# Optimization experiments

Hardware: AMD Instinct MI355X
Metric: run time of the kernel (lower is better)

## Reference

```python
import jax, jax.numpy as jnp
import numpy as np

EPS = 1e-9
N_HEAD = 16


def clamp_c(c):
    return jnp.clip(c, 1e-4, 1.0)


def _heads(x, H):
    B, T, C = x.shape
    return x.reshape(B, T, H, C // H)


def mobius_add(x, y, c_clamped, H):
    # per-head Mobius addition; c_clamped: (H,)
    B, T, C = x.shape
    cr = c_clamped.reshape(1, 1, H, 1)
    xr, yr = _heads(x, H), _heads(y, H)
    xn = jnp.sum(xr * xr, axis=-1, keepdims=True)
    yn = jnp.sum(yr * yr, axis=-1, keepdims=True)
    ip = jnp.sum(xr * yr, axis=-1, keepdims=True)
    num = (1 + 2 * cr * ip + cr * yn) * xr + (1 - cr * xn) * yr
    den = 1 + 2 * cr * ip + cr ** 2 * xn * yn
    return (num / (den + EPS)).reshape(B, T, C)


def expmap(x, v, c, H):
    # exponential map of tangent vector v at point x (per-head curvature)
    B, T, C = x.shape
    cc = clamp_c(c)
    cr = cc.reshape(1, 1, H, 1)
    xr, vr = _heads(x, H), _heads(v, H)
    sf = 2.0 / (1 + cr * jnp.sum(xr * xr, axis=-1, keepdims=True) + EPS)  # scaling factor
    vns = jnp.sum(vr * vr, axis=-1, keepdims=True)
    vn = jnp.sqrt(vns + EPS)
    tanh_arg = jnp.abs(cr * sf * vns / 2)
    coeff = (1.0 / (jnp.sqrt(jnp.abs(cr) + EPS) + EPS)) * jnp.tanh(jnp.sqrt(tanh_arg + EPS))
    second = (coeff * vr / (vn + EPS)).reshape(B, T, C)
    return mobius_add(x, second, cc, H)


def layernorm(x, g):
    m = jnp.mean(x, axis=-1, keepdims=True)
    v = jnp.mean((x - m) ** 2, axis=-1, keepdims=True)
    return (x - m) * jax.lax.rsqrt(v + 1e-5) * g


def attention(x, w_qkv, w_proj, H):
    B, T, C = x.shape
    hs = C // H
    q, k, v = jnp.split(x @ w_qkv.T, 3, axis=-1)
    q = q.reshape(B, T, H, hs).transpose(0, 2, 1, 3)
    k = k.reshape(B, T, H, hs).transpose(0, 2, 1, 3)
    v = v.reshape(B, T, H, hs).transpose(0, 2, 1, 3)
    att = jnp.einsum('bhqd,bhkd->bhqk', q, k) * (float(hs) ** -0.5)
    mask = jnp.tril(jnp.ones((T, T), dtype=bool))
    att = jnp.where(mask, att, -jnp.inf)
    att = jax.nn.softmax(att, axis=-1)
    y = jnp.einsum('bhqk,bhkd->bhqd', att, v)
    y = y.transpose(0, 2, 1, 3).reshape(B, T, C)
    return y @ w_proj.T


def setup_inputs() -> dict:
    key = jax.random.key(0)
    ks = jax.random.split(key, 9)
    B, T, C = 2, 2048, 1024
    s = 0.02
    return {
        'x': jax.random.normal(ks[0], (B, T, C), jnp.float32) * s,
        'ln1_g': jnp.ones((C,), jnp.float32),
        'w_qkv': jax.random.normal(ks[1], (3 * C, C), jnp.float32) * s,
        'w_attn_proj': jax.random.normal(ks[2], (C, C), jnp.float32) * s,
        'c_attn': jax.random.uniform(ks[3], (N_HEAD,), jnp.float32, 0.1, 0.9),
        'ln2_g': jnp.ones((C,), jnp.float32),
        'w_fc': jax.random.normal(ks[4], (4 * C, C), jnp.float32) * s,
        'w_mlp_proj': jax.random.normal(ks[5], (C, 4 * C), jnp.float32) * s,
        'c_mlp': jax.random.uniform(ks[6], (N_HEAD,), jnp.float32, 0.1, 0.9),
    }


def reference(x, ln1_g, w_qkv, w_attn_proj, c_attn, ln2_g, w_fc, w_mlp_proj, c_mlp):
    H = N_HEAD
    a = attention(layernorm(x, ln1_g), w_qkv, w_attn_proj, H)
    x = expmap(x, a, c_attn, H)  # hyperbolic residual (attn)
    h = jax.nn.gelu(layernorm(x, ln2_g) @ w_fc.T, approximate=False) @ w_mlp_proj.T
    x = expmap(x, h, c_mlp, H)   # hyperbolic residual (mlp)
    return x
```

## Files before the change

kernel.cpp:

```cpp
#include <hip/hip_runtime.h>
#include <hip/hip_bf16.h>

typedef __attribute__((ext_vector_type(8))) short bf16x8;
typedef __attribute__((ext_vector_type(4))) float f32x4;

typedef const __attribute__((address_space(1))) void gv_t;
typedef __attribute__((address_space(3))) void lv_t;
#define GLL16(g, l) __builtin_amdgcn_global_load_lds((gv_t*)(g), (lv_t*)(l), 16, 0, 0)

__device__ __forceinline__ short f2bf(float f) {
    __hip_bfloat16 h = __float2bfloat16(f);
    return *reinterpret_cast<short*>(&h);
}

__device__ __forceinline__ float wred(float v) {
    #pragma unroll
    for (int m = 1; m < 64; m <<= 1) v += __shfl_xor(v, m);
    return v;
}

__global__ __launch_bounds__(256) void cvt_kernel(const float* __restrict__ in,
                                                  short* __restrict__ out, int n4) {
    int i = blockIdx.x * 256 + threadIdx.x;
    if (i < n4) {
        float4 v = ((const float4*)in)[i];
        short4 o;
        o.x = f2bf(v.x); o.y = f2bf(v.y); o.z = f2bf(v.z); o.w = f2bf(v.w);
        ((short4*)out)[i] = o;
    }
}

__global__ __launch_bounds__(256) void ln_kernel(const float* __restrict__ x,
                                                 const float* __restrict__ g,
                                                 short* __restrict__ y) {
    const int row = blockIdx.x, tid = threadIdx.x;
    const float4 v = ((const float4*)(x + (size_t)row * 1024))[tid];
    float s = v.x + v.y + v.z + v.w;
    float s2 = v.x * v.x + v.y * v.y + v.z * v.z + v.w * v.w;
    #pragma unroll
    for (int m = 1; m < 64; m <<= 1) { s += __shfl_xor(s, m); s2 += __shfl_xor(s2, m); }
    __shared__ float rs[4], rs2[4];
    if ((tid & 63) == 0) { rs[tid >> 6] = s; rs2[tid >> 6] = s2; }
    __syncthreads();
    s = rs[0] + rs[1] + rs[2] + rs[3];
    s2 = rs2[0] + rs2[1] + rs2[2] + rs2[3];
    const float mean = s * (1.0f / 1024.0f);
    const float var = s2 * (1.0f / 1024.0f) - mean * mean;
    const float r = rsqrtf(var + 1e-5f);
    const float4 gg = ((const float4*)g)[tid];
    short4 o;
    o.x = f2bf((v.x - mean) * r * gg.x);
    o.y = f2bf((v.y - mean) * r * gg.y);
    o.z = f2bf((v.z - mean) * r * gg.z);
    o.w = f2bf((v.w - mean) * r * gg.w);
    ((short4*)y)[(size_t)row * 256 + tid] = o;
}

template <int EPI>
__global__ __launch_bounds__(256, 2) void gemm_bt(const short* __restrict__ A,
                                                  const short* __restrict__ Bw,
                                                  int M, int N, int K,
                                                  void* __restrict__ o0,
                                                  void* __restrict__ o1,
                                                  void* __restrict__ o2) {
    __shared__ __align__(16) short As[128 * 32];
    __shared__ __align__(16) short Bs[128 * 32];
    const int tid = threadIdx.x;
    const int wid = tid >> 6, lane = tid & 63;
    const int wm = wid >> 1, wn = wid & 1;
    const int col = lane & 15, grp = lane >> 4;
    const int m0 = blockIdx.x * 128, n0 = blockIdx.y * 128;
    f32x4 acc[4][4] = {};
    const int rowA = tid >> 2;
    const int kc = (tid & 3) * 8;
    const short* ga = A + (size_t)(m0 + rowA) * K + kc;
    const short* gb = Bw + (size_t)(n0 + rowA) * K + kc;
    short* lA = As + wid * 512;
    short* lB = Bs + wid * 512;
    for (int k0 = 0; k0 < K; k0 += 32) {
        GLL16(ga + k0, lA);
        GLL16(ga + k0 + (size_t)64 * K, lA + 2048);
        GLL16(gb + k0, lB);
        GLL16(gb + k0 + (size_t)64 * K, lB + 2048);
        __syncthreads();
        bf16x8 af[4], bfr[4];
        #pragma unroll
        for (int i = 0; i < 4; ++i) {
            af[i] = *(const bf16x8*)&As[(wm * 64 + i * 16 + col) * 32 + grp * 8];
            bfr[i] = *(const bf16x8*)&Bs[(wn * 64 + i * 16 + col) * 32 + grp * 8];
        }
        #pragma unroll
        for (int mi = 0; mi < 4; ++mi)
            #pragma unroll
            for (int ni = 0; ni < 4; ++ni)
                acc[mi][ni] = __builtin_amdgcn_mfma_f32_16x16x32_bf16(af[mi], bfr[ni], acc[mi][ni], 0, 0, 0);
        __syncthreads();
    }
    #pragma unroll
    for (int mi = 0; mi < 4; ++mi) {
        #pragma unroll
        for (int ni = 0; ni < 4; ++ni) {
            #pragma unroll
            for (int i = 0; i < 4; ++i) {
                const int m = m0 + wm * 64 + mi * 16 + grp * 4 + i;
                const int n = n0 + wn * 64 + ni * 16 + col;
                const float v = acc[mi][ni][i];
                if (EPI == 0) {
                    const int b = m >> 11, t = m & 2047;
                    const int which = n >> 10, nn = n & 1023;
                    const int h = nn >> 6, d = nn & 63;
                    const size_t bh = (size_t)(b * 16 + h);
                    if (which == 0)
                        ((short*)o0)[(bh * 2048 + t) * 64 + d] = f2bf(v * 0.125f);
                    else if (which == 1)
                        ((short*)o1)[(bh * 2048 + t) * 64 + d] = f2bf(v);
                    else
                        ((short*)o2)[(bh * 64 + d) * 2048 + t] = f2bf(v);
                } else if (EPI == 1) {
                    ((float*)o0)[(size_t)m * N + n] = v;
                } else {
                    const float gl = 0.5f * v * (1.0f + erff(v * 0.70710678118654752f));
                    ((short*)o0)[(size_t)m * N + n] = f2bf(gl);
                }
            }
        }
    }
}

__global__ __launch_bounds__(256, 3) void attn_kernel(const short* __restrict__ Q,
                                                      const short* __restrict__ Kg,
                                                      const short* __restrict__ VT,
                                                      short* __restrict__ Y) {
    __shared__ __align__(16) short Ks[2][4096];
    __shared__ __align__(16) short Vs[2][4096];
    __shared__ __align__(16) short Plds[4][16 * 72];
    const int j = 15 - blockIdx.x;
    const int bh = blockIdx.y;
    const int tid = threadIdx.x, wid = tid >> 6, lane = tid & 63;
    const int ql = lane & 15, g = lane >> 4;
    const int r8 = lane >> 3, s8 = lane & 7;
    const int q0w = j * 128 + wid * 32;
    const int lt = 2 * j + 1;
    const short* Qb = Q + (size_t)bh * 2048 * 64;
    const short* Kb = Kg + (size_t)bh * 2048 * 64;
    const short* Vb = VT + (size_t)bh * 64 * 2048;
    short* Pw = &Plds[wid][0];

    bf16x8 qf[2][2];
    #pragma unroll
    for (int qs = 0; qs < 2; ++qs) {
        qf[qs][0] = *(const bf16x8*)&Qb[(size_t)(q0w + 16 * qs + ql) * 64 + 8 * g];
        qf[qs][1] = *(const bf16x8*)&Qb[(size_t)(q0w + 16 * qs + ql) * 64 + 32 + 8 * g];
    }
    f32x4 o[2][4] = {};
    float m[2] = {-1e30f, -1e30f}, lsum[2] = {0.f, 0.f};

#define STAGE(b_, kt_) do {                                                      \
        const int kbase_ = (kt_) * 64;                                           \
        _Pragma("unroll")                                                        \
        for (int c = 0; c < 2; ++c) {                                            \
            const int row = c * 32 + wid * 8 + r8;                               \
            const int slot = s8 ^ (row & 7);                                     \
            GLL16(Kb + (size_t)(kbase_ + row) * 64 + slot * 8,                   \
                  (char*)&Ks[b_][0] + c * 4096 + wid * 1024);                    \
            GLL16(Vb + (size_t)row * 2048 + kbase_ + slot * 8,                   \
                  (char*)&Vs[b_][0] + c * 4096 + wid * 1024);                    \
        }                                                                        \
    } while (0)

    STAGE(0, 0);
    __syncthreads();
    int buf = 0;
    for (int kt = 0; kt <= lt; ++kt) {
        if (kt < lt) STAGE(buf ^ 1, kt + 1);
        const int kbase = kt * 64;
        const short* Kt = &Ks[buf][0];
        const short* Vt = &Vs[buf][0];
        bf16x8 kf[4][2];
        #pragma unroll
        for (int kb = 0; kb < 4; ++kb) {
            const int row = 16 * kb + ql;
            const int x = row & 7;
            kf[kb][0] = *(const bf16x8*)((const char*)Kt + row * 128 + ((g ^ x) << 4));
            kf[kb][1] = *(const bf16x8*)((const char*)Kt + row * 128 + (((4 + g) ^ x) << 4));
        }
        #pragma unroll
        for (int qs = 0; qs < 2; ++qs) {
            const int q0s = q0w + 16 * qs;
            if (kbase > q0s + 15) continue;
            f32x4 s[4];
            #pragma unroll
            for (int kb = 0; kb < 4; ++kb) {
                f32x4 z = {0.f, 0.f, 0.f, 0.f};
                z = __builtin_amdgcn_mfma_f32_16x16x32_bf16(kf[kb][0], qf[qs][0], z, 0, 0, 0);
                z = __builtin_amdgcn_mfma_f32_16x16x32_bf16(kf[kb][1], qf[qs][1], z, 0, 0, 0);
                s[kb] = z;
            }
            if (kbase + 63 > q0s) {
                #pragma unroll
                for (int kb = 0; kb < 4; ++kb)
                    #pragma unroll
                    for (int r = 0; r < 4; ++r)
                        if (kbase + 16 * kb + 4 * g + r > q0s + ql) s[kb][r] = -1e30f;
            }
            float t0 = fmaxf(fmaxf(s[0][0], s[0][1]), fmaxf(s[0][2], s[0][3]));
            float t1 = fmaxf(fmaxf(s[1][0], s[1][1]), fmaxf(s[1][2], s[1][3]));
            float t2 = fmaxf(fmaxf(s[2][0], s[2][1]), fmaxf(s[2][2], s[2][3]));
            float t3 = fmaxf(fmaxf(s[3][0], s[3][1]), fmaxf(s[3][2], s[3][3]));
            float tmax = fmaxf(fmaxf(t0, t1), fmaxf(t2, t3));
            tmax = fmaxf(tmax, __shfl_xor(tmax, 16));
            tmax = fmaxf(tmax, __shfl_xor(tmax, 32));
            const float mnew = fmaxf(m[qs], tmax);
            const float sc = __expf(m[qs] - mnew);
            m[qs] = mnew;
            float rsum = 0.0f;
            #pragma unroll
            for (int kb = 0; kb < 4; ++kb) {
                const float e0 = __expf(s[kb][0] - mnew);
                const float e1 = __expf(s[kb][1] - mnew);
                const float e2 = __expf(s[kb][2] - mnew);
                const float e3 = __expf(s[kb][3] - mnew);
                rsum += (e0 + e1) + (e2 + e3);
                short4 pk;
                pk.x = f2bf(e0); pk.y = f2bf(e1); pk.z = f2bf(e2); pk.w = f2bf(e3);
                *(short4*)&Pw[ql * 72 + 16 * kb + 4 * g] = pk;
            }
            rsum += __shfl_xor(rsum, 16);
            rsum += __shfl_xor(rsum, 32);
            lsum[qs] = lsum[qs] * sc + rsum;
            #pragma unroll
            for (int nf = 0; nf < 4; ++nf)
                #pragma unroll
                for (int r = 0; r < 4; ++r) o[qs][nf][r] *= sc;
            const bf16x8 pb0 = *(const bf16x8*)&Pw[ql * 72 + 8 * g];
            const bf16x8 pb1 = *(const bf16x8*)&Pw[ql * 72 + 32 + 8 * g];
            #pragma unroll
            for (int nf = 0; nf < 4; ++nf) {
                const int row = 16 * nf + ql;
                const int x = row & 7;
                bf16x8 v0 = *(const bf16x8*)((const char*)Vt + row * 128 + ((g ^ x) << 4));
                bf16x8 v1 = *(const bf16x8*)((const char*)Vt + row * 128 + (((4 + g) ^ x) << 4));
                o[qs][nf] = __builtin_amdgcn_mfma_f32_16x16x32_bf16(v0, pb0, o[qs][nf], 0, 0, 0);
                o[qs][nf] = __builtin_amdgcn_mfma_f32_16x16x32_bf16(v1, pb1, o[qs][nf], 0, 0, 0);
            }
        }
        __syncthreads();
        buf ^= 1;
    }
#undef STAGE
    const int b = bh >> 4, h = bh & 15;
    #pragma unroll
    for (int qs = 0; qs < 2; ++qs) {
        const float inv = 1.0f / lsum[qs];
        const size_t rowoff = ((size_t)b * 2048 + q0w + 16 * qs + ql) * 1024 + h * 64;
        #pragma unroll
        for (int nf = 0; nf < 4; ++nf) {
            short4 w;
            w.x = f2bf(o[qs][nf][0] * inv);
            w.y = f2bf(o[qs][nf][1] * inv);
            w.z = f2bf(o[qs][nf][2] * inv);
            w.w = f2bf(o[qs][nf][3] * inv);
            *(short4*)&Y[rowoff + 16 * nf + 4 * g] = w;
        }
    }
}

__global__ __launch_bounds__(256) void expmap_kernel(const float* __restrict__ x,
                                                     const float* __restrict__ v,
                                                     const float* __restrict__ carr,
                                                     float* __restrict__ out) {
    const int blk = blockIdx.x;
    const int row = blk >> 2;
    const int head = (blk & 3) * 4 + (threadIdx.x >> 6);
    const int lane = threadIdx.x & 63;
    const size_t idx = (size_t)row * 1024 + head * 64 + lane;
    float c = carr[head];
    c = fminf(fmaxf(c, 1e-4f), 1.0f);
    const float xe = x[idx], ve = v[idx];
    const float xn = wred(xe * xe);
    const float vns = wred(ve * ve);
    const float vn = sqrtf(vns + 1e-9f);
    const float sf = 2.0f / (1.0f + c * xn + 1e-9f);
    const float targ = fabsf(0.5f * c * sf * vns);
    const float coeff = (1.0f / (sqrtf(c + 1e-9f) + 1e-9f)) * tanhf(sqrtf(targ + 1e-9f));
    const float ye = coeff * ve / (vn + 1e-9f);
    const float yn = wred(ye * ye);
    const float ip = wred(xe * ye);
    const float num = (1.0f + 2.0f * c * ip + c * yn) * xe + (1.0f - c * xn) * ye;
    const float den = 1.0f + 2.0f * c * ip + c * c * xn * yn;
    out[idx] = num / (den + 1e-9f);
}

extern "C" void kernel_launch(void* const* d_in, const int* in_sizes, int n_in,
                              void* d_out, int out_size, void* d_ws, size_t ws_size,
                              hipStream_t stream) {
    (void)in_sizes; (void)n_in; (void)out_size; (void)ws_size;
    const float* x      = (const float*)d_in[0];
    const float* ln1_g  = (const float*)d_in[1];
    const float* w_qkv  = (const float*)d_in[2];
    const float* w_proj = (const float*)d_in[3];
    const float* c_attn = (const float*)d_in[4];
    const float* ln2_g  = (const float*)d_in[5];
    const float* w_fc   = (const float*)d_in[6];
    const float* w_mlp  = (const float*)d_in[7];
    const float* c_mlp  = (const float*)d_in[8];
    float* out = (float*)d_out;
    char* ws = (char*)d_ws;
    const size_t MB = 1024 * 1024;

    short* wqkv_bf  = (short*)(ws + 0 * MB);
    short* wproj_bf = (short*)(ws + 6 * MB);
    short* wfc_bf   = (short*)(ws + 8 * MB);
    short* wmlp_bf  = (short*)(ws + 16 * MB);
    short* y_bf     = (short*)(ws + 24 * MB);
    short* q_bf     = (short*)(ws + 32 * MB);
    short* k_bf     = (short*)(ws + 40 * MB);
    short* vT_bf    = (short*)(ws + 48 * MB);
    short* att_bf   = (short*)(ws + 56 * MB);
    float* a_f32    = (float*)(ws + 64 * MB);
    float* x1       = (float*)(ws + 80 * MB);
    short* g_bf     = (short*)(ws + 32 * MB);
    float* h_f32    = (float*)(ws + 64 * MB);

    cvt_kernel<<<3072, 256, 0, stream>>>(w_qkv, wqkv_bf, 3072 * 1024 / 4);
    cvt_kernel<<<1024, 256, 0, stream>>>(w_proj, wproj_bf, 1024 * 1024 / 4);
    cvt_kernel<<<4096, 256, 0, stream>>>(w_fc, wfc_bf, 4096 * 1024 / 4);
    cvt_kernel<<<4096, 256, 0, stream>>>(w_mlp, wmlp_bf, 1024 * 4096 / 4);

    ln_kernel<<<4096, 256, 0, stream>>>(x, ln1_g, y_bf);
    gemm_bt<0><<<dim3(32, 24), 256, 0, stream>>>(y_bf, wqkv_bf, 4096, 3072, 1024,
                                                 q_bf, k_bf, vT_bf);
    attn_kernel<<<dim3(16, 32), 256, 0, stream>>>(q_bf, k_bf, vT_bf, att_bf);
    gemm_bt<1><<<dim3(32, 8), 256, 0, stream>>>(att_bf, wproj_bf, 4096, 1024, 1024,
                                                a_f32, nullptr, nullptr);
    expmap_kernel<<<16384, 256, 0, stream>>>(x, a_f32, c_attn, x1);
    ln_kernel<<<4096, 256, 0, stream>>>(x1, ln2_g, y_bf);
    gemm_bt<2><<<dim3(32, 32), 256, 0, stream>>>(y_bf, wfc_bf, 4096, 4096, 1024,
                                                 g_bf, nullptr, nullptr);
    gemm_bt<1><<<dim3(32, 8), 256, 0, stream>>>(g_bf, wmlp_bf, 4096, 1024, 4096,
                                                h_f32, nullptr, nullptr);
    expmap_kernel<<<16384, 256, 0, stream>>>(x1, h_f32, c_mlp, out);
}
```

Measured before the change: 333.8 us.

## Double-buffer GEMM LDS tiles with K=64 stages and XOR-swizzled layout

Reworks the bf16 GEMM main loop to use two LDS buffers, so the next K-tile's global-to-LDS loads are issued before the current tile's MFMAs run, with one barrier per iteration instead of two. The K step grows from 32 to 64 and the LDS rows use an XOR swizzle on 16-byte slots to avoid bank conflicts on the fragment reads. LDS use rises to 64KB per block, which may reduce occupancy below the two blocks per CU the launch bounds request.

```diff
diff --git a/kernel.cpp b/kernel.cpp
--- a/kernel.cpp
+++ b/kernel.cpp
@@ -63,39 +63,59 @@
                                                   void* __restrict__ o0,
                                                   void* __restrict__ o1,
                                                   void* __restrict__ o2) {
-    __shared__ __align__(16) short As[128 * 32];
-    __shared__ __align__(16) short Bs[128 * 32];
+    __shared__ __align__(16) short As[2][128 * 64];
+    __shared__ __align__(16) short Bs[2][128 * 64];
     const int tid = threadIdx.x;
     const int wid = tid >> 6, lane = tid & 63;
     const int wm = wid >> 1, wn = wid & 1;
     const int col = lane & 15, grp = lane >> 4;
+    const int r8 = lane >> 3, s8 = lane & 7;
     const int m0 = blockIdx.x * 128, n0 = blockIdx.y * 128;
     f32x4 acc[4][4] = {};
-    const int rowA = tid >> 2;
-    const int kc = (tid & 3) * 8;
-    const short* ga = A + (size_t)(m0 + rowA) * K + kc;
-    const short* gb = Bw + (size_t)(n0 + rowA) * K + kc;
-    short* lA = As + wid * 512;
-    short* lB = Bs + wid * 512;
-    for (int k0 = 0; k0 < K; k0 += 32) {
-        GLL16(ga + k0, lA);
-        GLL16(ga + k0 + (size_t)64 * K, lA + 2048);
-        GLL16(gb + k0, lB);
-        GLL16(gb + k0 + (size_t)64 * K, lB + 2048);
+    const short* ga = A + (size_t)m0 * K;
+    const short* gb = Bw + (size_t)n0 * K;
+
+#define GSTAGE(b_, t_) do {                                                     \
+        const int k0_ = (t_) * 64;                                              \
+        _Pragma("unroll")                                                       \
+        for (int c = 0; c < 4; ++c) {                                           \
+            const int row = c * 32 + wid * 8 + r8;                              \
+            const int slot = s8 ^ (row & 7);                                    \
+            GLL16(ga + (size_t)row * K + k0_ + slot * 8,                        \
+                  (char*)&As[b_][0] + c * 4096 + wid * 1024);                   \
+            GLL16(gb + (size_t)row * K + k0_ + slot * 8,                        \
+                  (char*)&Bs[b_][0] + c * 4096 + wid * 1024);                   \
+        }                                                                       \
+    } while (0)
+
+    const int NT = K >> 6;
+    GSTAGE(0, 0);
+    __syncthreads();
+    int buf = 0;
+    for (int t = 0; t < NT; ++t) {
+        if (t + 1 < NT) GSTAGE(buf ^ 1, t + 1);
+        const char* At = (const char*)&As[buf][0];
+        const char* Bt = (const char*)&Bs[buf][0];
+        #pragma unroll
+        for (int s = 0; s < 2; ++s) {
+            bf16x8 af[4], bfr[4];
+            #pragma unroll
+            for (int i = 0; i < 4; ++i) {
+                const int rowA = wm * 64 + i * 16 + col;
+                const int rowB = wn * 64 + i * 16 + col;
+                af[i]  = *(const bf16x8*)(At + rowA * 128 + (((s * 4 + grp) ^ (rowA & 7)) << 4));
+                bfr[i] = *(const bf16x8*)(Bt + rowB * 128 + (((s * 4 + grp) ^ (rowB & 7)) << 4));
+            }
+            #pragma unroll
+            for (int mi = 0; mi < 4; ++mi)
+                #pragma unroll
+                for (int ni = 0; ni < 4; ++ni)
+                    acc[mi][ni] = __builtin_amdgcn_mfma_f32_16x16x32_bf16(af[mi], bfr[ni], acc[mi][ni], 0, 0, 0);
+        }
         __syncthreads();
-        bf16x8 af[4], bfr[4];
-        #pragma unroll
-        for (int i = 0; i < 4; ++i) {
-            af[i] = *(const bf16x8*)&As[(wm * 64 + i * 16 + col) * 32 + grp * 8];
-            bfr[i] = *(const bf16x8*)&Bs[(wn * 64 + i * 16 + col) * 32 + grp * 8];
-        }
-        #pragma unroll
-        for (int mi = 0; mi < 4; ++mi)
-            #pragma unroll
-            for (int ni = 0; ni < 4; ++ni)
-                acc[mi][ni] = __builtin_amdgcn_mfma_f32_16x16x32_bf16(af[mi], bfr[ni], acc[mi][ni], 0, 0, 0);
-        __syncthreads();
-    }
+        buf ^= 1;
+    }
+#undef GSTAGE
     #pragma unroll
     for (int mi = 0; mi < 4; ++mi) {
         #pragma unroll
```

Measured after the change: 311.0 us. 6.8% less time.
